# Performance work log

Measured on AMD Instinct MI355X. Metric: run time of the kernel, lower is better.

## Reference

```python
import jax, jax.numpy as jnp
import numpy as np

B, S, E = 2, 2048, 1024
H = 16
D = E // H
LAYER_IDX = 2.0
MASKED_BIAS = -10000.0


def setup_inputs() -> dict:
    key = jax.random.key(0)
    k1, k2, k3 = jax.random.split(key, 3)
    hidden_state = jax.random.normal(k1, (B, S, E), dtype=jnp.float32)
    w_attn = jax.random.normal(k2, (E, 3 * E), dtype=jnp.float32) * 0.2
    b_attn = jnp.zeros((3 * E,), dtype=jnp.float32)
    w_proj = jax.random.normal(k3, (E, E), dtype=jnp.float32) * 0.2
    b_proj = jnp.zeros((E,), dtype=jnp.float32)
    return {"hidden_state": hidden_state, "w_attn": w_attn, "b_attn": b_attn,
            "w_proj": w_proj, "b_proj": b_proj}


def reference(hidden_state, w_attn, b_attn, w_proj, b_proj):
    b, s, e = hidden_state.shape
    # c_attn: Conv1D == x @ W + b, then split into q, k, v
    qkv = hidden_state @ w_attn + b_attn          # [b, s, 3E]
    q, k, v = jnp.split(qkv, 3, axis=-1)
    # split heads -> [b, H, s, D]
    def split_heads(t):
        return t.reshape(b, s, H, D).transpose(0, 2, 1, 3)
    q, k, v = split_heads(q), split_heads(k), split_heads(v)
    # QK^T scaled by sqrt(d_head) then by layer_idx
    scores = jnp.einsum("bhqd,bhkd->bhqk", q, k)
    scores = scores / jnp.asarray(D ** 0.5, scores.dtype)
    scores = scores / LAYER_IDX
    # causal mask with masked_bias fill (-10000.0), matching bias buffer slice
    causal = jnp.tril(jnp.ones((s, s), dtype=bool))  # [s, s]
    scores = jnp.where(causal[None, None, :, :], scores, jnp.asarray(MASKED_BIAS, scores.dtype))
    attn = jax.nn.softmax(scores, axis=-1)
    out = jnp.einsum("bhqk,bhkd->bhqd", attn, v)   # [b, H, s, D]
    # merge heads
    out = out.transpose(0, 2, 1, 3).reshape(b, s, e)
    # c_proj
    return out @ w_proj + b_proj
```

## Files before the change

kernel.cpp:

```cpp
#include <hip/hip_runtime.h>
#include <cstddef>
#include <cstdint>

#define B_DIM   2
#define S_LEN   2048
#define EMB     1024
#define NH      16
#define HD      64
#define QKV_N   3072
#define MROWS   (B_DIM * S_LEN)

using half8  = __attribute__((ext_vector_type(8))) _Float16;
using half4  = __attribute__((ext_vector_type(4))) _Float16;
using f32x4  = __attribute__((ext_vector_type(4))) float;

#if defined(__has_builtin)
#if __has_builtin(__builtin_amdgcn_global_load_lds)
#define HAS_GLL 1
#endif
#endif

__device__ __forceinline__ void stage16(const _Float16* g, _Float16* lds_base, int lane)
{
#ifdef HAS_GLL
    (void)lane;
    __builtin_amdgcn_global_load_lds(
        (const __attribute__((address_space(1))) unsigned int*)g,
        (__attribute__((address_space(3))) unsigned int*)lds_base, 16, 0, 0);
#else
    *(half8*)(lds_base + lane * 8) = *(const half8*)g;
#endif
}

__global__ __launch_bounds__(256)
void cast_f32_f16(const float* __restrict__ src, _Float16* __restrict__ dst)
{
    int i = (blockIdx.x * 256 + threadIdx.x) * 4;
    float4 v = *(const float4*)(src + i);
    half4 h = { (_Float16)v.x, (_Float16)v.y, (_Float16)v.z, (_Float16)v.w };
    *(half4*)(dst + i) = h;
}

__global__ __launch_bounds__(256)
void transpose_cast(const float* __restrict__ W, _Float16* __restrict__ Wt,
                    int K, int N)
{
    __shared__ float T[32][33];
    const int n0 = blockIdx.x * 32, k0 = blockIdx.y * 32;
    const int t = threadIdx.x;
    const int r = t >> 3, c4 = (t & 7) * 4;
    float4 w = *(const float4*)(W + (size_t)(k0 + r) * N + n0 + c4);
    T[r][c4 + 0] = w.x; T[r][c4 + 1] = w.y;
    T[r][c4 + 2] = w.z; T[r][c4 + 3] = w.w;
    __syncthreads();
    half4 h = { (_Float16)T[c4 + 0][r], (_Float16)T[c4 + 1][r],
                (_Float16)T[c4 + 2][r], (_Float16)T[c4 + 3][r] };
    *(half4*)(Wt + (size_t)(n0 + r) * K + k0 + c4) = h;
}

__global__ __launch_bounds__(256)
void transpose_v(const _Float16* __restrict__ qkv, _Float16* __restrict__ vt)
{
    __shared__ _Float16 T[64][66];
    const int st = blockIdx.x, bh = blockIdx.y;
    const int b = bh >> 4, h = bh & 15;
    const int t = threadIdx.x;
    const int sr = t >> 2, dc = (t & 3) * 16;

    const _Float16* src = qkv + ((size_t)(b * S_LEN + st * 64 + sr)) * QKV_N
                              + 2 * EMB + h * HD + dc;
    half8 v0 = *(const half8*)(src);
    half8 v1 = *(const half8*)(src + 8);
#pragma unroll
    for (int j = 0; j < 8; ++j) { T[sr][dc + j] = v0[j]; T[sr][dc + 8 + j] = v1[j]; }
    __syncthreads();

    const int dr = t >> 2, sc = (t & 3) * 16;
    half8 o0, o1;
#pragma unroll
    for (int j = 0; j < 8; ++j) { o0[j] = T[sc + j][dr]; o1[j] = T[sc + 8 + j][dr]; }
    _Float16* dst = vt + (size_t)bh * HD * S_LEN + (size_t)dr * S_LEN + st * 64 + sc;
    *(half8*)(dst)     = o0;
    *(half8*)(dst + 8) = o1;
}

template <int MT, int MINW, bool OUT_F16>
__global__ __launch_bounds__(256, MINW)
void hgemm_lds(const _Float16* __restrict__ X, const _Float16* __restrict__ Wt,
               const float* __restrict__ bias, void* __restrict__ Cout,
               int M, int N, int K)
{
    constexpr int BM = MT * 32;
    constexpr int ACALLS = BM / 32;
    __shared__ _Float16 As[BM][64];
    __shared__ _Float16 Bs[128][64];

    const int tid  = threadIdx.x;
    const int wave = tid >> 6, lane = tid & 63;
    const int quad = lane >> 4, l15 = lane & 15;
    const int wm = (wave >> 1) * (MT * 16);
    const int wn = (wave & 1) * 64;
    const int m0 = blockIdx.y * BM, n0 = blockIdx.x * 128;

    const int srow = lane >> 3;
    const int scol = ((lane & 7) ^ srow) * 8;

    const _Float16* xg[ACALLS];
#pragma unroll
    for (int c = 0; c < ACALLS; ++c)
        xg[c] = X + (size_t)(m0 + wave * (BM / 4) + c * 8 + srow) * K + scol;
    const _Float16* wg[4];
#pragma unroll
    for (int c = 0; c < 4; ++c)
        wg[c] = Wt + (size_t)(n0 + wave * 32 + c * 8 + srow) * K + scol;

    f32x4 acc[MT][4] = {};
    const int sx = l15 & 7;

    for (int k0 = 0; k0 < K; k0 += 64) {
#pragma unroll
        for (int c = 0; c < ACALLS; ++c)
            stage16(xg[c] + k0, &As[wave * (BM / 4) + c * 8][0], lane);
#pragma unroll
        for (int c = 0; c < 4; ++c)
            stage16(wg[c] + k0, &Bs[wave * 32 + c * 8][0], lane);
        __syncthreads();

#pragma unroll
        for (int cc = 0; cc < 2; ++cc) {
            half8 af[MT], bf[4];
#pragma unroll
            for (int mt = 0; mt < MT; ++mt)
                af[mt] = *(const half8*)&As[wm + mt * 16 + l15][(((cc * 4 + quad) ^ sx)) * 8];
#pragma unroll
            for (int nt = 0; nt < 4; ++nt)
                bf[nt] = *(const half8*)&Bs[wn + nt * 16 + l15][(((cc * 4 + quad) ^ sx)) * 8];
#pragma unroll
            for (int mt = 0; mt < MT; ++mt)
#pragma unroll
                for (int nt = 0; nt < 4; ++nt)
                    acc[mt][nt] = __builtin_amdgcn_mfma_f32_16x16x32_f16(
                        af[mt], bf[nt], acc[mt][nt], 0, 0, 0);
        }
        __syncthreads();
    }

#pragma unroll
    for (int nt = 0; nt < 4; ++nt) {
        const int c = n0 + wn + nt * 16 + l15;
        const float bv = bias[c];
#pragma unroll
        for (int mt = 0; mt < MT; ++mt)
#pragma unroll
            for (int reg = 0; reg < 4; ++reg) {
                const int r = m0 + wm + mt * 16 + quad * 4 + reg;
                const float v = acc[mt][nt][reg] + bv;
                if (OUT_F16)
                    ((_Float16*)Cout)[(size_t)r * N + c] = (_Float16)v;
                else
                    ((float*)Cout)[(size_t)r * N + c] = v;
            }
    }
}

__global__ __launch_bounds__(256, 4)
void attn_fa_mfma5(const _Float16* __restrict__ qkv,
                   const _Float16* __restrict__ vt,
                   _Float16* __restrict__ outh)
{
    __shared__ _Float16 Ks[128][64];
    __shared__ _Float16 Vs[64][128];

    const int n    = blockIdx.x;
    const int half = n >> 9, idx = n & 511;
    const int bh   = idx >> 4, jj = idx & 15;
    const int qt   = half ? (31 - jj) : jj;
    const int b = bh >> 4, h = bh & 15;

    const int tid  = threadIdx.x;
    const int wave = tid >> 6, lane = tid & 63;
    const int quad = lane >> 4, l15 = lane & 15;
    const size_t row0 = (size_t)b * S_LEN;

    const _Float16 qscale = (_Float16)0.0901684400555602f;
    half8 qf[2];
    {
        const size_t qrow = row0 + qt * 64 + wave * 16 + l15;
        const _Float16* qp = qkv + qrow * QKV_N + h * HD + quad * 8;
#pragma unroll
        for (int c = 0; c < 2; ++c) {
            half8 q = *(const half8*)(qp + c * 32);
#pragma unroll
            for (int j = 0; j < 8; ++j) q[j] = q[j] * qscale;
            qf[c] = q;
        }
    }

    f32x4 o_acc[4] = {};
    float m_i = -1e30f, l_i = 0.0f;

    const int ksrow = lane >> 3;
    const int kscol = ((lane & 7) ^ ksrow) * 8;
    const int vsrow = lane >> 4;
    const _Float16* vbase = vt + (size_t)bh * HD * S_LEN;
    const int sxk = l15 & 7;

    const int ktN = (qt + 2) >> 1;
    for (int kt = 0; kt < ktN; ++kt) {
        __syncthreads();
        {
            const _Float16* kbase = qkv + (row0 + kt * 128) * QKV_N + EMB + h * HD;
#pragma unroll
            for (int c = 0; c < 4; ++c) {
                const int r0 = wave * 32 + c * 8;
                stage16(kbase + (size_t)(r0 + ksrow) * QKV_N + kscol,
                        &Ks[r0][0], lane);
            }
#pragma unroll
            for (int c = 0; c < 4; ++c) {
                const int r0 = wave * 16 + c * 4;
                const int sgv = ((lane & 15) ^ (c * 4 + vsrow)) * 8;
                stage16(vbase + (size_t)(r0 + vsrow) * S_LEN + kt * 128 + sgv,
                        &Vs[r0][0], lane);
            }
        }
        __syncthreads();

        f32x4 st[8] = {};
#pragma unroll
        for (int c = 0; c < 2; ++c)
#pragma unroll
            for (int nt = 0; nt < 8; ++nt) {
                half8 kf = *(const half8*)&Ks[nt * 16 + l15][((c * 4 + quad) ^ sxk) * 8];
                st[nt] = __builtin_amdgcn_mfma_f32_16x16x32_f16(kf, qf[c], st[nt], 0, 0, 0);
            }

        if (kt == ktN - 1) {
            const int q = qt * 64 + wave * 16 + l15;
#pragma unroll
            for (int nt = 0; nt < 8; ++nt) {
                const int ks = kt * 128 + nt * 16 + quad * 4;
#pragma unroll
                for (int reg = 0; reg < 4; ++reg)
                    if (ks + reg > q) st[nt][reg] = -1e30f;
            }
        }

        float rm = fmaxf(fmaxf(st[0][0], st[0][1]), fmaxf(st[0][2], st[0][3]));
#pragma unroll
        for (int nt = 1; nt < 8; ++nt) {
            rm = fmaxf(rm, fmaxf(st[nt][0], st[nt][1]));
            rm = fmaxf(rm, fmaxf(st[nt][2], st[nt][3]));
        }
        rm = fmaxf(rm, __shfl_xor(rm, 16));
        rm = fmaxf(rm, __shfl_xor(rm, 32));
        const float mnew = fmaxf(m_i, rm);

        if (__ballot(mnew > m_i)) {
            const float alpha = __builtin_amdgcn_exp2f(m_i - mnew);
            l_i *= alpha;
#pragma unroll
            for (int dt = 0; dt < 4; ++dt)
#pragma unroll
                for (int reg = 0; reg < 4; ++reg) o_acc[dt][reg] *= alpha;
        }
        m_i = mnew;

        float rs = 0.0f;
        half4 pf[8];
#pragma unroll
        for (int nt = 0; nt < 8; ++nt) {
            float p0 = __builtin_amdgcn_exp2f(st[nt][0] - mnew);
            float p1 = __builtin_amdgcn_exp2f(st[nt][1] - mnew);
            float p2 = __builtin_amdgcn_exp2f(st[nt][2] - mnew);
            float p3 = __builtin_amdgcn_exp2f(st[nt][3] - mnew);
            rs += (p0 + p1) + (p2 + p3);
            pf[nt] = half4{ (_Float16)p0, (_Float16)p1, (_Float16)p2, (_Float16)p3 };
        }
        rs += __shfl_xor(rs, 16);
        rs += __shfl_xor(rs, 32);
        l_i += rs;

#pragma unroll
        for (int nt = 0; nt < 8; ++nt)
#pragma unroll
            for (int dt = 0; dt < 4; ++dt) {
                const int pg = ((2 * nt + (quad >> 1)) ^ l15) * 8 + (quad & 1) * 4;
                half4 vf = *(const half4*)&Vs[dt * 16 + l15][pg];
                o_acc[dt] = __builtin_amdgcn_mfma_f32_16x16x16f16(vf, pf[nt], o_acc[dt], 0, 0, 0);
            }
    }

    const float inv = 1.0f / l_i;
    const size_t r = row0 + qt * 64 + wave * 16 + l15;
#pragma unroll
    for (int dt = 0; dt < 4; ++dt) {
        half4 o = { (_Float16)(o_acc[dt][0] * inv), (_Float16)(o_acc[dt][1] * inv),
                    (_Float16)(o_acc[dt][2] * inv), (_Float16)(o_acc[dt][3] * inv) };
        *(half4*)(outh + r * EMB + h * HD + dt * 16 + quad * 4) = o;
    }
}

extern "C" void kernel_launch(void* const* d_in, const int* in_sizes, int n_in,
                              void* d_out, int out_size, void* d_ws, size_t ws_size,
                              hipStream_t stream)
{
    const float* hidden = (const float*)d_in[0];
    const float* w_attn = (const float*)d_in[1];
    const float* b_attn = (const float*)d_in[2];
    const float* w_proj = (const float*)d_in[3];
    const float* b_proj = (const float*)d_in[4];

    _Float16* hidden_h = (_Float16*)d_ws;
    _Float16* wattn_t  = hidden_h + (size_t)MROWS * EMB;
    _Float16* wproj_t  = wattn_t + (size_t)EMB * QKV_N;
    _Float16* qkv_h    = wproj_t + (size_t)EMB * EMB;
    _Float16* attn_h   = qkv_h + (size_t)MROWS * QKV_N;
    _Float16* vt       = attn_h + (size_t)MROWS * EMB;

    cast_f32_f16<<<(MROWS * EMB) / 1024, 256, 0, stream>>>(hidden, hidden_h);
    transpose_cast<<<dim3(QKV_N / 32, EMB / 32), 256, 0, stream>>>(
        w_attn, wattn_t, EMB, QKV_N);
    transpose_cast<<<dim3(EMB / 32, EMB / 32), 256, 0, stream>>>(
        w_proj, wproj_t, EMB, EMB);

    hgemm_lds<4, 3, true><<<dim3(QKV_N / 128, MROWS / 128), 256, 0, stream>>>(
        hidden_h, wattn_t, b_attn, qkv_h, MROWS, QKV_N, EMB);

    transpose_v<<<dim3(S_LEN / 64, B_DIM * NH), 256, 0, stream>>>(qkv_h, vt);

    attn_fa_mfma5<<<dim3(1024), 256, 0, stream>>>(qkv_h, vt, attn_h);

    hgemm_lds<2, 4, false><<<dim3(EMB / 128, MROWS / 64), 256, 0, stream>>>(
        attn_h, wproj_t, b_proj, d_out, MROWS, EMB, EMB);
}
```

Baseline: 188.9 us.

## Merge prep kernels, fuse V transpose into QKV GEMM epilogue, remap attention blocks per XCD

Merges the three cast/transpose prep kernels into one launch. The QKV GEMM epilogue now writes the V columns directly in transposed per-head layout, which removes the separate transpose_v kernel and its extra read and write of V. The attention grid mapping is changed so consecutive block IDs spread over the 8 XCDs, giving each XCD four heads and interleaving causal work. Costs are fewer launches and less traffic, against strided half4 stores in the V epilogue.

```diff
diff --git a/kernel.cpp b/kernel.cpp
--- a/kernel.cpp
+++ b/kernel.cpp
@@ -33,21 +33,26 @@
 }
 
 __global__ __launch_bounds__(256)
-void cast_f32_f16(const float* __restrict__ src, _Float16* __restrict__ dst)
-{
-    int i = (blockIdx.x * 256 + threadIdx.x) * 4;
-    float4 v = *(const float4*)(src + i);
-    half4 h = { (_Float16)v.x, (_Float16)v.y, (_Float16)v.z, (_Float16)v.w };
-    *(half4*)(dst + i) = h;
-}
-
-__global__ __launch_bounds__(256)
-void transpose_cast(const float* __restrict__ W, _Float16* __restrict__ Wt,
-                    int K, int N)
-{
+void prep_all(const float* __restrict__ hidden, const float* __restrict__ w_attn,
+              const float* __restrict__ w_proj, _Float16* __restrict__ hidden_h,
+              _Float16* __restrict__ wattn_t, _Float16* __restrict__ wproj_t)
+{
+    const int bid = blockIdx.x, t = threadIdx.x;
+    if (bid < 4096) {
+        int i = bid * 1024 + t * 4;
+        float4 v = *(const float4*)(hidden + i);
+        half4 h = { (_Float16)v.x, (_Float16)v.y, (_Float16)v.z, (_Float16)v.w };
+        *(half4*)(hidden_h + i) = h;
+        return;
+    }
     __shared__ float T[32][33];
-    const int n0 = blockIdx.x * 32, k0 = blockIdx.y * 32;
-    const int t = threadIdx.x;
+    const float* W; _Float16* Wt; int N, bx, by;
+    if (bid < 7168) {
+        int t2 = bid - 4096; bx = t2 % 96; by = t2 / 96; W = w_attn; Wt = wattn_t; N = QKV_N;
+    } else {
+        int t3 = bid - 7168; bx = t3 & 31; by = t3 >> 5; W = w_proj; Wt = wproj_t; N = EMB;
+    }
+    const int n0 = bx * 32, k0 = by * 32;
     const int r = t >> 3, c4 = (t & 7) * 4;
     float4 w = *(const float4*)(W + (size_t)(k0 + r) * N + n0 + c4);
     T[r][c4 + 0] = w.x; T[r][c4 + 1] = w.y;
@@ -55,40 +60,14 @@
     __syncthreads();
     half4 h = { (_Float16)T[c4 + 0][r], (_Float16)T[c4 + 1][r],
                 (_Float16)T[c4 + 2][r], (_Float16)T[c4 + 3][r] };
-    *(half4*)(Wt + (size_t)(n0 + r) * K + k0 + c4) = h;
-}
-
-__global__ __launch_bounds__(256)
-void transpose_v(const _Float16* __restrict__ qkv, _Float16* __restrict__ vt)
-{
-    __shared__ _Float16 T[64][66];
-    const int st = blockIdx.x, bh = blockIdx.y;
-    const int b = bh >> 4, h = bh & 15;
-    const int t = threadIdx.x;
-    const int sr = t >> 2, dc = (t & 3) * 16;
-
-    const _Float16* src = qkv + ((size_t)(b * S_LEN + st * 64 + sr)) * QKV_N
-                              + 2 * EMB + h * HD + dc;
-    half8 v0 = *(const half8*)(src);
-    half8 v1 = *(const half8*)(src + 8);
-#pragma unroll
-    for (int j = 0; j < 8; ++j) { T[sr][dc + j] = v0[j]; T[sr][dc + 8 + j] = v1[j]; }
-    __syncthreads();
-
-    const int dr = t >> 2, sc = (t & 3) * 16;
-    half8 o0, o1;
-#pragma unroll
-    for (int j = 0; j < 8; ++j) { o0[j] = T[sc + j][dr]; o1[j] = T[sc + 8 + j][dr]; }
-    _Float16* dst = vt + (size_t)bh * HD * S_LEN + (size_t)dr * S_LEN + st * 64 + sc;
-    *(half8*)(dst)     = o0;
-    *(half8*)(dst + 8) = o1;
-}
-
-template <int MT, int MINW, bool OUT_F16>
+    *(half4*)(Wt + (size_t)(n0 + r) * EMB + k0 + c4) = h;
+}
+
+template <int MT, int MINW, bool OUT_F16, bool FUSE_VT>
 __global__ __launch_bounds__(256, MINW)
 void hgemm_lds(const _Float16* __restrict__ X, const _Float16* __restrict__ Wt,
                const float* __restrict__ bias, void* __restrict__ Cout,
-               int M, int N, int K)
+               _Float16* __restrict__ vt, int M, int N, int K)
 {
     constexpr int BM = MT * 32;
     constexpr int ACALLS = BM / 32;
@@ -143,6 +122,25 @@
                         af[mt], bf[nt], acc[mt][nt], 0, 0, 0);
         }
         __syncthreads();
+    }
+
+    if (FUSE_VT && n0 >= 2 * EMB) {
+#pragma unroll
+        for (int nt = 0; nt < 4; ++nt) {
+            const int c  = n0 + wn + nt * 16 + l15;
+            const float bv = bias[c];
+            const int vcol = c - 2 * EMB;
+            const int hh = vcol >> 6, dd = vcol & 63;
+#pragma unroll
+            for (int mt = 0; mt < MT; ++mt) {
+                const int r = m0 + wm + mt * 16 + quad * 4;
+                const int bb = r >> 11, ss = r & 2047;
+                half4 o = { (_Float16)(acc[mt][nt][0] + bv), (_Float16)(acc[mt][nt][1] + bv),
+                            (_Float16)(acc[mt][nt][2] + bv), (_Float16)(acc[mt][nt][3] + bv) };
+                *(half4*)(vt + ((size_t)(bb * NH + hh) * HD + dd) * S_LEN + ss) = o;
+            }
+        }
+        return;
     }
 
 #pragma unroll
@@ -164,17 +162,17 @@
 }
 
 __global__ __launch_bounds__(256, 4)
-void attn_fa_mfma5(const _Float16* __restrict__ qkv,
+void attn_fa_mfma6(const _Float16* __restrict__ qkv,
                    const _Float16* __restrict__ vt,
                    _Float16* __restrict__ outh)
 {
     __shared__ _Float16 Ks[128][64];
     __shared__ _Float16 Vs[64][128];
 
-    const int n    = blockIdx.x;
-    const int half = n >> 9, idx = n & 511;
-    const int bh   = idx >> 4, jj = idx & 15;
-    const int qt   = half ? (31 - jj) : jj;
+    const int n   = blockIdx.x;
+    const int xcd = n & 7, g = (n >> 3) & 3, j = n >> 5;
+    const int bh  = xcd * 4 + g;
+    const int qt  = (j < 16) ? j : (47 - j);
     const int b = bh >> 4, h = bh & 15;
 
     const int tid  = threadIdx.x;
@@ -191,7 +189,7 @@
         for (int c = 0; c < 2; ++c) {
             half8 q = *(const half8*)(qp + c * 32);
 #pragma unroll
-            for (int j = 0; j < 8; ++j) q[j] = q[j] * qscale;
+            for (int j2 = 0; j2 < 8; ++j2) q[j2] = q[j2] * qscale;
             qf[c] = q;
         }
     }
@@ -318,19 +316,14 @@
     _Float16* attn_h   = qkv_h + (size_t)MROWS * QKV_N;
     _Float16* vt       = attn_h + (size_t)MROWS * EMB;
 
-    cast_f32_f16<<<(MROWS * EMB) / 1024, 256, 0, stream>>>(hidden, hidden_h);
-    transpose_cast<<<dim3(QKV_N / 32, EMB / 32), 256, 0, stream>>>(
-        w_attn, wattn_t, EMB, QKV_N);
-    transpose_cast<<<dim3(EMB / 32, EMB / 32), 256, 0, stream>>>(
-        w_proj, wproj_t, EMB, EMB);
-
-    hgemm_lds<4, 3, true><<<dim3(QKV_N / 128, MROWS / 128), 256, 0, stream>>>(
-        hidden_h, wattn_t, b_attn, qkv_h, MROWS, QKV_N, EMB);
-
-    transpose_v<<<dim3(S_LEN / 64, B_DIM * NH), 256, 0, stream>>>(qkv_h, vt);
-
-    attn_fa_mfma5<<<dim3(1024), 256, 0, stream>>>(qkv_h, vt, attn_h);
-
-    hgemm_lds<2, 4, false><<<dim3(EMB / 128, MROWS / 64), 256, 0, stream>>>(
-        attn_h, wproj_t, b_proj, d_out, MROWS, EMB, EMB);
-}
+    prep_all<<<8192, 256, 0, stream>>>(hidden, w_attn, w_proj,
+                                       hidden_h, wattn_t, wproj_t);
+
+    hgemm_lds<4, 3, true, true><<<dim3(QKV_N / 128, MROWS / 128), 256, 0, stream>>>(
+        hidden_h, wattn_t, b_attn, qkv_h, vt, MROWS, QKV_N, EMB);
+
+    attn_fa_mfma6<<<dim3(1024), 256, 0, stream>>>(qkv_h, vt, attn_h);
+
+    hgemm_lds<2, 4, false, false><<<dim3(EMB / 128, MROWS / 64), 256, 0, stream>>>(
+        attn_h, wproj_t, b_proj, d_out, nullptr, MROWS, EMB, EMB);
+}
```

Measured after the change: 183.7 us. 2.7% less time.
